# Kernel tuning notes

Hardware: AMD Instinct MI355X
Metric: run time of the kernel (lower is better)

Reference implementation:

```python
import jax, jax.numpy as jnp
import numpy as np


def setup_inputs() -> dict:
    key = jax.random.key(0)
    k1, k2 = jax.random.split(key)
    B, C, T = 32, 64, 8192
    y_pred = jax.random.normal(k1, (B, C, T), dtype=jnp.float32)
    y_true = jax.random.normal(k2, (B, C, T), dtype=jnp.float32)
    return {"y_pred": y_pred, "y_true": y_true}


def reference(y_pred, y_true):
    # Faithful to the torch code: the triu mask multiply + sum over the second
    # time axis is exactly abs_diff[b,c,t] weighted by row-sum of triu = (T - t).
    # channel_sums then sums over t and c; final reduction is a mean over batch.
    B, C, T = y_pred.shape
    abs_diff = jnp.abs(y_pred - y_true)                      # (B, C, T)
    w = jnp.arange(T, 0, -1, dtype=abs_diff.dtype)           # weight[t] = T - t
    per_batch = jnp.einsum('bct,t->b', abs_diff, w)          # (B,)
    scaling = 2.0 / (T * C * (T + 1))                        # apply_scaling_factor=True
    return scaling * jnp.mean(per_batch)
```

## Files before the change

kernel.cpp:

```cpp
#include <hip/hip_runtime.h>


#define T_MASK 8191
#define T_DIMF 8192.0f

#define FLOATS_PER_BLOCK 8192
#define CHUNK_FLOATS 4096
#define NITER (FLOATS_PER_BLOCK / CHUNK_FLOATS)

typedef float vfloat4 __attribute__((ext_vector_type(4)));

__device__ __forceinline__ void load_lds16(const float* g, float* l) {
    __builtin_amdgcn_global_load_lds(
        (const __attribute__((address_space(1))) void*)g,
        (__attribute__((address_space(3))) void*)l,
        16 , 0 , 0 );
}

__global__ __launch_bounds__(256)
void wl_partial_kernel(const float* __restrict__ a,
                       const float* __restrict__ b,
                       float* __restrict__ partial) {
    __shared__ float ldsB[CHUNK_FLOATS];

    const int tid  = threadIdx.x;
    const int lane = tid & 63;
    const int wave = tid >> 6;
    const int blockBase = blockIdx.x * FLOATS_PER_BLOCK;

    float acc = 0.0f;

    for (int it = 0; it < NITER; ++it) {
        const int chunkBase = blockBase + it * CHUNK_FLOATS;

        #pragma unroll
        for (int s = 0; s < 4; ++s) {
            const int seg = wave * 1024 + s * 256;
            load_lds16(b + chunkBase + seg + lane * 4, &ldsB[seg]);
        }

        vfloat4 xa[4];
        const vfloat4* a4 = (const vfloat4*)a;
        const int c4 = chunkBase >> 2;
        #pragma unroll
        for (int k = 0; k < 4; ++k)
            xa[k] = __builtin_nontemporal_load(&a4[c4 + tid + k * 256]);

        __syncthreads();

        #pragma unroll
        for (int k = 0; k < 4; ++k) {
            const int f4 = tid + k * 256;
            vfloat4 y = ((const vfloat4*)ldsB)[f4];
            const int g = chunkBase + f4 * 4;
            float w = T_DIMF - (float)(g & T_MASK);
            float d0 = fabsf(xa[k].x - y.x);
            float d1 = fabsf(xa[k].y - y.y);
            float d2 = fabsf(xa[k].z - y.z);
            float d3 = fabsf(xa[k].w - y.w);
            acc += w * (d0 + d1 + d2 + d3) - (d1 + 2.0f * d2 + 3.0f * d3);
        }
        __syncthreads();
    }

    #pragma unroll
    for (int off = 32; off > 0; off >>= 1)
        acc += __shfl_down(acc, off, 64);

    __shared__ float wave_sums[4];
    if (lane == 0) wave_sums[wave] = acc;
    __syncthreads();

    if (tid == 0)
        partial[blockIdx.x] = wave_sums[0] + wave_sums[1] + wave_sums[2] + wave_sums[3];
}

__global__ __launch_bounds__(256)
void wl_final_kernel(const float* __restrict__ partial, int n,
                     float* __restrict__ out, float scale) {
    float acc = 0.0f;
    for (int i = threadIdx.x; i < n; i += 256)
        acc += partial[i];

    #pragma unroll
    for (int off = 32; off > 0; off >>= 1)
        acc += __shfl_down(acc, off, 64);

    __shared__ float wave_sums[4];
    int lane = threadIdx.x & 63;
    int wave = threadIdx.x >> 6;
    if (lane == 0) wave_sums[wave] = acc;
    __syncthreads();

    if (threadIdx.x == 0)
        out[0] = (wave_sums[0] + wave_sums[1] + wave_sums[2] + wave_sums[3]) * scale;
}

extern "C" void kernel_launch(void* const* d_in, const int* in_sizes, int n_in,
                              void* d_out, int out_size, void* d_ws, size_t ws_size,
                              hipStream_t stream) {
    const float* a = (const float*)d_in[0];
    const float* b = (const float*)d_in[1];
    float* out = (float*)d_out;
    float* partial = (float*)d_ws;

    int n = in_sizes[0];
    int blocks = n / FLOATS_PER_BLOCK;

    const long long T = 8192;
    const long long C = 64;
    const long long B = (long long)n / (C * T);
    float scale = (float)(2.0 / ((double)T * (double)C * (double)(T + 1) * (double)B));

    wl_partial_kernel<<<blocks, 256, 0, stream>>>(a, b, partial);
    wl_final_kernel<<<1, 256, 0, stream>>>(partial, blocks, out, scale);
}
```

Before: 131.1 us.

## Offload last eighth of each block's data to scalar-unit loads

New measurement: 147.9 us. 1.13x slower.

```diff
diff --git a/kernel.cpp b/kernel.cpp
--- a/kernel.cpp
+++ b/kernel.cpp
@@ -3,12 +3,10 @@
 
 #define T_MASK 8191
 #define T_DIMF 8192.0f
-
 #define FLOATS_PER_BLOCK 8192
-#define CHUNK_FLOATS 4096
-#define NITER (FLOATS_PER_BLOCK / CHUNK_FLOATS)
 
 typedef float vfloat4 __attribute__((ext_vector_type(4)));
+typedef float sfloat16 __attribute__((ext_vector_type(16)));
 
 __device__ __forceinline__ void load_lds16(const float* g, float* l) {
     __builtin_amdgcn_global_load_lds(
@@ -17,21 +15,55 @@
         16 , 0 , 0 );
 }
 
+__device__ __forceinline__ sfloat16 sload16(const float* p, unsigned byte_off) {
+    sfloat16 x;
+    asm volatile("s_load_dwordx16 %0, %1, %2"
+                 : "=s"(x)
+                 : "s"(p), "s"(byte_off));
+    return x;
+}
+
+__device__ __forceinline__ void swait_lgkm0() {
+    asm volatile("s_waitcnt lgkmcnt(0)" ::: "memory");
+    __builtin_amdgcn_sched_barrier(0);
+}
+
+__device__ __forceinline__ float scalar_round(const float* a, const float* b,
+                                              unsigned off, float wbase) {
+    sfloat16 x0 = sload16(a, off);
+    sfloat16 x1 = sload16(a, off + 64u);
+    sfloat16 y0 = sload16(b, off);
+    sfloat16 y1 = sload16(b, off + 64u);
+    swait_lgkm0();
+    float s = 0.0f;
+    #pragma unroll
+    for (int j = 0; j < 16; ++j) {
+        s += (wbase - (float)j)        * fabsf(x0[j] - y0[j]);
+        s += (wbase - (float)(16 + j)) * fabsf(x1[j] - y1[j]);
+    }
+    return s;
+}
+
 __global__ __launch_bounds__(256)
 void wl_partial_kernel(const float* __restrict__ a,
                        const float* __restrict__ b,
                        float* __restrict__ partial) {
-    __shared__ float ldsB[CHUNK_FLOATS];
+    __shared__ float ldsB[4096];
 
     const int tid  = threadIdx.x;
     const int lane = tid & 63;
     const int wave = tid >> 6;
+    const int wq   = __builtin_amdgcn_readfirstlane(wave);
     const int blockBase = blockIdx.x * FLOATS_PER_BLOCK;
 
-    float acc = 0.0f;
+    float acc  = 0.0f;
+    float accS = 0.0f;
 
-    for (int it = 0; it < NITER; ++it) {
-        const int chunkBase = blockBase + it * CHUNK_FLOATS;
+    const vfloat4* a4 = (const vfloat4*)a;
+    const unsigned sbase = (unsigned)(blockBase + 7168 + wq * 256) * 4u;
+
+    {
+        const int chunkBase = blockBase;
 
         #pragma unroll
         for (int s = 0; s < 4; ++s) {
@@ -40,11 +72,16 @@
         }
 
         vfloat4 xa[4];
-        const vfloat4* a4 = (const vfloat4*)a;
         const int c4 = chunkBase >> 2;
         #pragma unroll
         for (int k = 0; k < 4; ++k)
             xa[k] = __builtin_nontemporal_load(&a4[c4 + tid + k * 256]);
+
+        #pragma unroll
+        for (int r = 0; r < 4; ++r) {
+            const float wbase = (float)(1024 - wq * 256 - r * 32);
+            accS += scalar_round(a, b, sbase + (unsigned)r * 128u, wbase);
+        }
 
         __syncthreads();
 
@@ -62,6 +99,45 @@
         }
         __syncthreads();
     }
+
+    {
+        const int chunkBase = blockBase + 4096;
+
+        #pragma unroll
+        for (int s = 0; s < 3; ++s) {
+            const int seg = wave * 768 + s * 256;
+            load_lds16(b + chunkBase + seg + lane * 4, &ldsB[seg]);
+        }
+
+        vfloat4 xa[3];
+        const int c4 = chunkBase >> 2;
+        #pragma unroll
+        for (int k = 0; k < 3; ++k)
+            xa[k] = __builtin_nontemporal_load(&a4[c4 + tid + k * 256]);
+
+        #pragma unroll
+        for (int r = 4; r < 8; ++r) {
+            const float wbase = (float)(1024 - wq * 256 - r * 32);
+            accS += scalar_round(a, b, sbase + (unsigned)r * 128u, wbase);
+        }
+
+        __syncthreads();
+
+        #pragma unroll
+        for (int k = 0; k < 3; ++k) {
+            const int f4 = tid + k * 256;
+            vfloat4 y = ((const vfloat4*)ldsB)[f4];
+            const int g = chunkBase + f4 * 4;
+            float w = T_DIMF - (float)(g & T_MASK);
+            float d0 = fabsf(xa[k].x - y.x);
+            float d1 = fabsf(xa[k].y - y.y);
+            float d2 = fabsf(xa[k].z - y.z);
+            float d3 = fabsf(xa[k].w - y.w);
+            acc += w * (d0 + d1 + d2 + d3) - (d1 + 2.0f * d2 + 3.0f * d3);
+        }
+    }
+
+    acc += accS * 0.015625f;
 
     #pragma unroll
     for (int off = 32; off > 0; off >>= 1)
```
